# Performance work log

Measured on AMD Instinct MI355X. Metric: run time of the kernel, lower is better.

The kernel has to match this reference:

```python
import jax, jax.numpy as jnp
import numpy as np

L, H, FF, NH = 6, 1024, 4096, 8
HD = H // NH
B, S = 4, 1024
EPS = 1e-5


def _fp8_roundtrip(w):
    # matches torch path: cast to float8_e4m3fn and back (done once at init, no grad)
    return w.astype(jnp.float8_e4m3fn).astype(w.dtype)


def setup_inputs() -> dict:
    key = jax.random.key(0)
    ks = jax.random.split(key, 6)
    x = jax.random.normal(ks[0], (B, S, H), dtype=jnp.float32)
    sH = 1.0 / np.sqrt(H)
    sF = 1.0 / np.sqrt(FF)
    qkv_w = _fp8_roundtrip(jax.random.normal(ks[1], (L, 3 * H, H), jnp.float32) * sH)
    proj_w = _fp8_roundtrip(jax.random.normal(ks[2], (L, H, H), jnp.float32) * sH)
    fc1_w = _fp8_roundtrip(jax.random.normal(ks[3], (L, FF, H), jnp.float32) * sH)
    fc2_w = _fp8_roundtrip(jax.random.normal(ks[4], (L, H, FF), jnp.float32) * sF)
    return {
        "x": x,
        "qkv_w": qkv_w, "qkv_b": jnp.zeros((L, 3 * H), jnp.float32),
        "proj_w": proj_w, "proj_b": jnp.zeros((L, H), jnp.float32),
        "fc1_w": fc1_w, "fc1_b": jnp.zeros((L, FF), jnp.float32),
        "fc2_w": fc2_w, "fc2_b": jnp.zeros((L, H), jnp.float32),
        "ln1_s": jnp.ones((L, H), jnp.float32), "ln1_b": jnp.zeros((L, H), jnp.float32),
        "ln2_s": jnp.ones((L, H), jnp.float32), "ln2_b": jnp.zeros((L, H), jnp.float32),
    }


def _layernorm(x, scale, bias):
    mu = jnp.mean(x, axis=-1, keepdims=True)
    var = jnp.var(x, axis=-1, keepdims=True)
    return (x - mu) / jnp.sqrt(var + EPS) * scale + bias


def reference(x, qkv_w, qkv_b, proj_w, proj_b, fc1_w, fc1_b, fc2_w, fc2_b,
              ln1_s, ln1_b, ln2_s, ln2_b):
    b, s, h = x.shape
    for i in range(L):
        # --- attention block ---
        residual = x
        hx = _layernorm(x, ln1_s[i], ln1_b[i])
        qkv = hx @ qkv_w[i].T + qkv_b[i]                       # [b, s, 3h]
        q, k, v = jnp.split(qkv, 3, axis=-1)
        q = q.reshape(b, s, NH, HD).transpose(0, 2, 1, 3)      # [b, nh, s, hd]
        k = k.reshape(b, s, NH, HD).transpose(0, 2, 1, 3)
        v = v.reshape(b, s, NH, HD).transpose(0, 2, 1, 3)
        scores = jnp.einsum('bhqd,bhkd->bhqk', q, k) / np.sqrt(HD)
        attn = jax.nn.softmax(scores, axis=-1)
        out = jnp.einsum('bhqk,bhkd->bhqd', attn, v)           # [b, nh, s, hd]
        out = out.transpose(0, 2, 1, 3).reshape(b, s, h)
        x = out @ proj_w[i].T + proj_b[i] + residual
        # --- FFN block ---
        residual = x
        hx = _layernorm(x, ln2_s[i], ln2_b[i])
        ff = jax.nn.relu(hx @ fc1_w[i].T + fc1_b[i])
        x = ff @ fc2_w[i].T + fc2_b[i] + residual
    return x
```

## Files before the change

### kernel.cpp

```cpp
#include <hip/hip_runtime.h>
#include <stdint.h>

typedef __bf16 bf16;
typedef __bf16 bf16x4 __attribute__((ext_vector_type(4)));
typedef __bf16 bf16x8 __attribute__((ext_vector_type(8)));
typedef float  f32x4  __attribute__((ext_vector_type(4)));

#define NLAYER 6
#define HDIM   1024
#define FFDIM  4096
#define NHEAD  8
#define HEADD  128
#define SEQ    1024
#define NTOK   4096

__device__ __forceinline__ void g2l16(const void* g, void* l) {
  __builtin_amdgcn_global_load_lds(
      (const __attribute__((address_space(1))) void*)g,
      (__attribute__((address_space(3))) void*)l, 16, 0, 0);
}

__global__ __launch_bounds__(256) void cvt_w(const float* __restrict__ in,
                                             bf16* __restrict__ out, int n8) {
  int i = blockIdx.x * 256 + threadIdx.x;
  if (i >= n8) return;
  const f32x4* p = (const f32x4*)in + (size_t)i * 2;
  f32x4 a = p[0], b = p[1];
  bf16x8 o;
  o[0] = (bf16)a[0]; o[1] = (bf16)a[1]; o[2] = (bf16)a[2]; o[3] = (bf16)a[3];
  o[4] = (bf16)b[0]; o[5] = (bf16)b[1]; o[6] = (bf16)b[2]; o[7] = (bf16)b[3];
  *((bf16x8*)out + i) = o;
}

__global__ __launch_bounds__(256) void ln_k(const float* __restrict__ x,
                                            const float* __restrict__ sc,
                                            const float* __restrict__ bi,
                                            bf16* __restrict__ out) {
  int row = blockIdx.x, t = threadIdx.x;
  f32x4 v = *((const f32x4*)(x + (size_t)row * HDIM) + t);
  float s = v[0] + v[1] + v[2] + v[3];
  float q = v[0]*v[0] + v[1]*v[1] + v[2]*v[2] + v[3]*v[3];
#pragma unroll
  for (int m = 1; m < 64; m <<= 1) {
    s += __shfl_xor(s, m, 64);
    q += __shfl_xor(q, m, 64);
  }
  __shared__ float ss[4], qq[4];
  if ((t & 63) == 0) { ss[t >> 6] = s; qq[t >> 6] = q; }
  __syncthreads();
  s = ss[0] + ss[1] + ss[2] + ss[3];
  q = qq[0] + qq[1] + qq[2] + qq[3];
  float mu  = s * (1.f / HDIM);
  float var = q * (1.f / HDIM) - mu * mu;
  float rs  = rsqrtf(var + 1e-5f);
  f32x4 g = *((const f32x4*)sc + t);
  f32x4 b = *((const f32x4*)bi + t);
  bf16x4 o;
#pragma unroll
  for (int j = 0; j < 4; j++) o[j] = (bf16)((v[j] - mu) * rs * g[j] + b[j]);
  *((bf16x4*)(out + (size_t)row * HDIM) + t) = o;
}

template <bool RELU, bool RESID, bool OUTF32, bool SPLITV>
__global__ __launch_bounds__(256) void gemm5(const bf16* __restrict__ A,
                                             const bf16* __restrict__ W,
                                             const float* __restrict__ bias,
                                             const float* resid, void* outp,
                                             bf16* __restrict__ vt,
                                             int M, int N, int K) {
  __shared__ bf16 As[2][128 * 64];
  __shared__ bf16 Bs[2][128 * 64];
  int tid = threadIdx.x;
  int lane = tid & 63, w = tid >> 6;
  int g = lane >> 4, r = lane & 15;
  int wr = w >> 1, wc = w & 1;
  int nbx = N >> 7;
  int cpx = gridDim.x >> 3;
  int swz = (blockIdx.x & 7) * cpx + (blockIdx.x >> 3);
  int bm = swz / nbx, bn = swz % nbx;
  const bf16* Ab = A + (size_t)bm * 128 * K;
  const bf16* Wb = W + (size_t)bn * 128 * K;
  f32x4 acc[4][4] = {};

  auto STAGE = [&](int buf, int k0) {
#pragma unroll
    for (int i = 0; i < 4; ++i) {
      int c = i * 256 + tid;
      int row = c >> 3;
      int kk = ((c & 7) ^ (row & 7)) << 3;
      g2l16(Ab + (size_t)row * K + k0 + kk, (char*)As[buf] + c * 16);
      g2l16(Wb + (size_t)row * K + k0 + kk, (char*)Bs[buf] + c * 16);
    }
  };
  auto COMPUTE = [&](int buf) {
#pragma unroll
    for (int ks = 0; ks < 2; ++ks) {
      bf16x8 af[4], bfr[4];
#pragma unroll
      for (int mi = 0; mi < 4; mi++) {
        int row = wr * 64 + mi * 16 + r;
        af[mi] = *(const bf16x8*)((const char*)As[buf] + row * 128 +
                                  ((ks * 64 + g * 16) ^ ((row & 7) << 4)));
      }
#pragma unroll
      for (int ni = 0; ni < 4; ni++) {
        int row = wc * 64 + ni * 16 + r;
        bfr[ni] = *(const bf16x8*)((const char*)Bs[buf] + row * 128 +
                                   ((ks * 64 + g * 16) ^ ((row & 7) << 4)));
      }
      __builtin_amdgcn_s_setprio(1);
#pragma unroll
      for (int mi = 0; mi < 4; mi++)
#pragma unroll
        for (int ni = 0; ni < 4; ni++)
          acc[mi][ni] = __builtin_amdgcn_mfma_f32_16x16x32_bf16(
              af[mi], bfr[ni], acc[mi][ni], 0, 0, 0);
      __builtin_amdgcn_s_setprio(0);
    }
  };

  int nt = K >> 6;
  STAGE(0, 0);
  __syncthreads();
  int cur = 0;
  for (int t = 0; t < nt - 1; ++t) {
    STAGE(cur ^ 1, (t + 1) << 6);
    COMPUTE(cur);
    __syncthreads();
    cur ^= 1;
  }
  COMPUTE(cur);

#pragma unroll
  for (int ni = 0; ni < 4; ++ni) {
    int col = bn * 128 + wc * 64 + ni * 16 + r;
    float bv = bias[col];
    bool vpart = SPLITV && (bn * 128 + wc * 64 + ni * 16) >= 2048;
    if (vpart) {
      int hh = (col - 2048) >> 7, dd = col & 127;
#pragma unroll
      for (int mi = 0; mi < 4; ++mi) {
        int row0 = bm * 128 + wr * 64 + mi * 16 + g * 4;
        int bb = row0 >> 10, ss = row0 & 1023;
        bf16x4 o;
#pragma unroll
        for (int j = 0; j < 4; j++) o[j] = (bf16)(acc[mi][ni][j] + bv);
        *(bf16x4*)(vt + ((size_t)((bb * NHEAD + hh) * HEADD + dd)) * SEQ + ss) = o;
      }
    } else {
#pragma unroll
      for (int mi = 0; mi < 4; ++mi) {
        int row0 = bm * 128 + wr * 64 + mi * 16 + g * 4;
#pragma unroll
        for (int j = 0; j < 4; j++) {
          size_t idx = (size_t)(row0 + j) * N + col;
          float v = acc[mi][ni][j] + bv;
          if constexpr (RELU) v = fmaxf(v, 0.f);
          if constexpr (RESID) v += resid[idx];
          if constexpr (OUTF32) ((float*)outp)[idx] = v;
          else                  ((bf16*)outp)[idx] = (bf16)v;
        }
      }
    }
  }
  (void)M;
}

__global__ __launch_bounds__(256) void attn_k(const bf16* __restrict__ qkv,
                                              const bf16* __restrict__ vt,
                                              bf16* __restrict__ out) {
  __shared__ bf16 Ks[64 * 128];
  __shared__ bf16 VT[128 * 64];
  __shared__ bf16 Ps[4][1024];
  int qt = blockIdx.x, h = blockIdx.y, b = blockIdx.z;
  int tid = threadIdx.x, lane = tid & 63, w = tid >> 6;
  int g = lane >> 4, r = lane & 15;
  int q0 = qt * 64;
  size_t tok0 = (size_t)b * SEQ;
  char* psw = (char*)Ps + w * 2048;

  bf16x8 qf[4];
  {
    const bf16* qp = qkv + (tok0 + q0 + w * 16 + r) * 3072 + h * HEADD;
#pragma unroll
    for (int ks = 0; ks < 4; ks++) qf[ks] = *(const bf16x8*)(qp + ks * 32 + g * 8);
  }
  f32x4 oacc[8] = {};
  float mprev[4], lsum[4];
#pragma unroll
  for (int j = 0; j < 4; j++) { mprev[j] = -1e30f; lsum[j] = 0.f; }
  const float scl = 0.08838834764831845f;
  const bf16* vtb = vt + (size_t)(b * NHEAD + h) * HEADD * SEQ;

  for (int c0 = 0; c0 < SEQ; c0 += 64) {
    const bf16* kbase = qkv + (tok0 + c0) * 3072 + 1024 + h * HEADD;
#pragma unroll
    for (int i = 0; i < 4; i++) {
      int cb = i * 256 + w * 64;
      int c  = cb + lane;
      int krow = c >> 4;
      int kkk  = ((c & 15) ^ (krow & 7)) << 3;
      g2l16(kbase + (size_t)krow * 3072 + kkk, (char*)Ks + cb * 16);
      int vrow = c >> 3;
      int vcol = ((c & 7) ^ (vrow & 7)) << 3;
      g2l16(vtb + (size_t)vrow * SEQ + c0 + vcol, (char*)VT + cb * 16);
    }
    __syncthreads();

    f32x4 sacc[4] = {};
#pragma unroll
    for (int ks = 0; ks < 4; ks++) {
#pragma unroll
      for (int cb = 0; cb < 4; cb++) {
        int row = cb * 16 + r;
        bf16x8 kf = *(const bf16x8*)((const char*)Ks + row * 256 +
                                     ((ks * 64 + g * 16) ^ ((row & 7) << 4)));
        sacc[cb] = __builtin_amdgcn_mfma_f32_16x16x32_bf16(qf[ks], kf, sacc[cb], 0, 0, 0);
      }
    }
#pragma unroll
    for (int cb = 0; cb < 4; cb++) {
      sacc[cb][0] *= scl; sacc[cb][1] *= scl; sacc[cb][2] *= scl; sacc[cb][3] *= scl;
    }
    float sf[4];
#pragma unroll
    for (int j = 0; j < 4; j++) {
      float m = fmaxf(fmaxf(sacc[0][j], sacc[1][j]), fmaxf(sacc[2][j], sacc[3][j]));
      m = fmaxf(m, __shfl_xor(m, 1, 64));
      m = fmaxf(m, __shfl_xor(m, 2, 64));
      m = fmaxf(m, __shfl_xor(m, 4, 64));
      m = fmaxf(m, __shfl_xor(m, 8, 64));
      float mn = fmaxf(mprev[j], m);
      float f  = __expf(mprev[j] - mn);
      mprev[j] = mn; sf[j] = f;
      float rs = 0.f;
#pragma unroll
      for (int cb = 0; cb < 4; cb++) {
        float p = __expf(sacc[cb][j] - mn);
        sacc[cb][j] = p; rs += p;
      }
      rs += __shfl_xor(rs, 1, 64);
      rs += __shfl_xor(rs, 2, 64);
      rs += __shfl_xor(rs, 4, 64);
      rs += __shfl_xor(rs, 8, 64);
      lsum[j] = lsum[j] * f + rs;
    }
#pragma unroll
    for (int nb = 0; nb < 8; nb++) {
      oacc[nb][0] *= sf[0]; oacc[nb][1] *= sf[1];
      oacc[nb][2] *= sf[2]; oacc[nb][3] *= sf[3];
    }
#pragma unroll
    for (int cb = 0; cb < 4; cb++) {
      int cbyte = cb * 32 + r * 2;
#pragma unroll
      for (int j = 0; j < 4; j++) {
        int q = g * 4 + j;
        *(bf16*)(psw + q * 128 + (cbyte ^ ((q & 7) << 4))) = (bf16)sacc[cb][j];
      }
    }
    asm volatile("s_waitcnt lgkmcnt(0)" ::: "memory");
    __builtin_amdgcn_sched_barrier(0);
#pragma unroll
    for (int cs = 0; cs < 2; cs++) {
      bf16x8 pf = *(const bf16x8*)(psw + r * 128 + ((cs * 64 + g * 16) ^ ((r & 7) << 4)));
#pragma unroll
      for (int nb = 0; nb < 8; nb++) {
        int vrow = nb * 16 + r;
        bf16x8 vf = *(const bf16x8*)((const char*)VT + vrow * 128 +
                                     ((cs * 64 + g * 16) ^ ((vrow & 7) << 4)));
        oacc[nb] = __builtin_amdgcn_mfma_f32_16x16x32_bf16(pf, vf, oacc[nb], 0, 0, 0);
      }
    }
    __syncthreads();
  }

  float rl[4];
#pragma unroll
  for (int j = 0; j < 4; j++) rl[j] = 1.f / lsum[j];
#pragma unroll
  for (int nb = 0; nb < 8; nb++)
#pragma unroll
    for (int j = 0; j < 4; j++)
      out[(tok0 + q0 + w * 16 + g * 4 + j) * HDIM + h * HEADD + nb * 16 + r] =
          (bf16)(oacc[nb][j] * rl[j]);
}

extern "C" void kernel_launch(void* const* d_in, const int* in_sizes, int n_in,
                              void* d_out, int out_size, void* d_ws, size_t ws_size,
                              hipStream_t stream) {
  const float* x_in   = (const float*)d_in[0];
  const float* qkv_w  = (const float*)d_in[1];
  const float* qkv_b  = (const float*)d_in[2];
  const float* proj_w = (const float*)d_in[3];
  const float* proj_b = (const float*)d_in[4];
  const float* fc1_w  = (const float*)d_in[5];
  const float* fc1_b  = (const float*)d_in[6];
  const float* fc2_w  = (const float*)d_in[7];
  const float* fc2_b  = (const float*)d_in[8];
  const float* ln1_s  = (const float*)d_in[9];
  const float* ln1_b  = (const float*)d_in[10];
  const float* ln2_s  = (const float*)d_in[11];
  const float* ln2_b  = (const float*)d_in[12];

  char* ws = (char*)d_ws;
  size_t o = 0;
  bf16* Wq = (bf16*)(ws + o); o += (size_t)NLAYER * 3 * HDIM * HDIM * 2;
  bf16* Wp = (bf16*)(ws + o); o += (size_t)NLAYER * HDIM * HDIM * 2;
  bf16* W1 = (bf16*)(ws + o); o += (size_t)NLAYER * FFDIM * HDIM * 2;
  bf16* W2 = (bf16*)(ws + o); o += (size_t)NLAYER * HDIM * FFDIM * 2;
  bf16* hx   = (bf16*)(ws + o); o += (size_t)NTOK * HDIM * 2;
  bf16* qkvb = (bf16*)(ws + o); o += (size_t)NTOK * 3 * HDIM * 2;
  bf16* Vt   = (bf16*)(ws + o); o += (size_t)NTOK * HDIM * 2;
  bf16* aout = (bf16*)(ws + o); o += (size_t)NTOK * HDIM * 2;
  bf16* ffb  = (bf16*)(ws + o); o += (size_t)NTOK * FFDIM * 2;
  float* xbuf = (float*)d_out;

  {
    int n8;
    n8 = NLAYER * 3 * HDIM * HDIM / 8;
    cvt_w<<<(n8 + 255) / 256, 256, 0, stream>>>(qkv_w, Wq, n8);
    n8 = NLAYER * HDIM * HDIM / 8;
    cvt_w<<<(n8 + 255) / 256, 256, 0, stream>>>(proj_w, Wp, n8);
    n8 = NLAYER * FFDIM * HDIM / 8;
    cvt_w<<<(n8 + 255) / 256, 256, 0, stream>>>(fc1_w, W1, n8);
    n8 = NLAYER * HDIM * FFDIM / 8;
    cvt_w<<<(n8 + 255) / 256, 256, 0, stream>>>(fc2_w, W2, n8);
  }

  for (int i = 0; i < NLAYER; i++) {
    const float* xc = (i == 0) ? x_in : xbuf;
    ln_k<<<NTOK, 256, 0, stream>>>(xc, ln1_s + i * HDIM, ln1_b + i * HDIM, hx);
    gemm5<false, false, false, true><<<(NTOK / 128) * (3 * HDIM / 128), 256, 0, stream>>>(
        hx, Wq + (size_t)i * 3 * HDIM * HDIM, qkv_b + i * 3 * HDIM, nullptr,
        qkvb, Vt, NTOK, 3 * HDIM, HDIM);
    attn_k<<<dim3(SEQ / 64, NHEAD, 4), 256, 0, stream>>>(qkvb, Vt, aout);
    gemm5<false, true, true, false><<<(NTOK / 128) * (HDIM / 128), 256, 0, stream>>>(
        aout, Wp + (size_t)i * HDIM * HDIM, proj_b + i * HDIM, xc,
        xbuf, nullptr, NTOK, HDIM, HDIM);
    ln_k<<<NTOK, 256, 0, stream>>>(xbuf, ln2_s + i * HDIM, ln2_b + i * HDIM, hx);
    gemm5<true, false, false, false><<<(NTOK / 128) * (FFDIM / 128), 256, 0, stream>>>(
        hx, W1 + (size_t)i * FFDIM * HDIM, fc1_b + i * FFDIM, nullptr,
        ffb, nullptr, NTOK, FFDIM, HDIM);
    gemm5<false, true, true, false><<<(NTOK / 128) * (HDIM / 128), 256, 0, stream>>>(
        ffb, W2 + (size_t)i * HDIM * FFDIM, fc2_b + i * HDIM, xbuf,
        xbuf, nullptr, NTOK, HDIM, FFDIM);
  }
  (void)in_sizes; (void)n_in; (void)out_size; (void)ws_size;
}
```

Measured before the change: 1.835 ms.

## Split GEMM K dimension across two warp groups within a block

The GEMM block grows to 512 threads, and each 256-thread half processes half of the K range with its own double-buffered LDS tiles. The two partial accumulators are then reduced through LDS, and only the first half runs the epilogue. The goal is more waves per tile to hide latency, especially for small-grid GEMMs like the proj and fc2 launches. In exchange, LDS use doubles to 128KB per block, occupancy drops, and the reduction and epilogue add serialized work.

Result: no change. 1.808 ms (-1.4%).

```diff
diff --git a/kernel.cpp b/kernel.cpp
--- a/kernel.cpp
+++ b/kernel.cpp
@@ -62,18 +62,21 @@
 }
 
 template <bool RELU, bool RESID, bool OUTF32, bool SPLITV>
-__global__ __launch_bounds__(256) void gemm5(const bf16* __restrict__ A,
-                                             const bf16* __restrict__ W,
-                                             const float* __restrict__ bias,
-                                             const float* resid, void* outp,
-                                             bf16* __restrict__ vt,
-                                             int M, int N, int K) {
-  __shared__ bf16 As[2][128 * 64];
-  __shared__ bf16 Bs[2][128 * 64];
+__global__ __launch_bounds__(512) void gemmsk(const bf16* __restrict__ A,
+                                              const bf16* __restrict__ W,
+                                              const float* __restrict__ bias,
+                                              const float* resid, void* outp,
+                                              bf16* __restrict__ vt,
+                                              int M, int N, int K) {
+  __shared__ bf16 As[2][2][128 * 64];
+  __shared__ bf16 Bs[2][2][128 * 64];
   int tid = threadIdx.x;
-  int lane = tid & 63, w = tid >> 6;
+  int gr = tid >> 8;
+  int gtid = tid & 255;
+  int lane = tid & 63;
+  int w4 = gtid >> 6;
   int g = lane >> 4, r = lane & 15;
-  int wr = w >> 1, wc = w & 1;
+  int wr = w4 >> 1, wc = w4 & 1;
   int nbx = N >> 7;
   int cpx = gridDim.x >> 3;
   int swz = (blockIdx.x & 7) * cpx + (blockIdx.x >> 3);
@@ -85,11 +88,11 @@
   auto STAGE = [&](int buf, int k0) {
 #pragma unroll
     for (int i = 0; i < 4; ++i) {
-      int c = i * 256 + tid;
+      int c = i * 256 + gtid;
       int row = c >> 3;
       int kk = ((c & 7) ^ (row & 7)) << 3;
-      g2l16(Ab + (size_t)row * K + k0 + kk, (char*)As[buf] + c * 16);
-      g2l16(Wb + (size_t)row * K + k0 + kk, (char*)Bs[buf] + c * 16);
+      g2l16(Ab + (size_t)row * K + k0 + kk, (char*)As[gr][buf] + c * 16);
+      g2l16(Wb + (size_t)row * K + k0 + kk, (char*)Bs[gr][buf] + c * 16);
     }
   };
   auto COMPUTE = [&](int buf) {
@@ -99,13 +102,13 @@
 #pragma unroll
       for (int mi = 0; mi < 4; mi++) {
         int row = wr * 64 + mi * 16 + r;
-        af[mi] = *(const bf16x8*)((const char*)As[buf] + row * 128 +
+        af[mi] = *(const bf16x8*)((const char*)As[gr][buf] + row * 128 +
                                   ((ks * 64 + g * 16) ^ ((row & 7) << 4)));
       }
 #pragma unroll
       for (int ni = 0; ni < 4; ni++) {
         int row = wc * 64 + ni * 16 + r;
-        bfr[ni] = *(const bf16x8*)((const char*)Bs[buf] + row * 128 +
+        bfr[ni] = *(const bf16x8*)((const char*)Bs[gr][buf] + row * 128 +
                                    ((ks * 64 + g * 16) ^ ((row & 7) << 4)));
       }
       __builtin_amdgcn_s_setprio(1);
@@ -119,46 +122,65 @@
     }
   };
 
-  int nt = K >> 6;
-  STAGE(0, 0);
+  int kbase = gr * (K >> 1);
+  int nt = K >> 7;
+  STAGE(0, kbase);
   __syncthreads();
   int cur = 0;
   for (int t = 0; t < nt - 1; ++t) {
-    STAGE(cur ^ 1, (t + 1) << 6);
+    STAGE(cur ^ 1, kbase + ((t + 1) << 6));
     COMPUTE(cur);
     __syncthreads();
     cur ^= 1;
   }
   COMPUTE(cur);
 
-#pragma unroll
-  for (int ni = 0; ni < 4; ++ni) {
-    int col = bn * 128 + wc * 64 + ni * 16 + r;
-    float bv = bias[col];
-    bool vpart = SPLITV && (bn * 128 + wc * 64 + ni * 16) >= 2048;
-    if (vpart) {
-      int hh = (col - 2048) >> 7, dd = col & 127;
-#pragma unroll
-      for (int mi = 0; mi < 4; ++mi) {
-        int row0 = bm * 128 + wr * 64 + mi * 16 + g * 4;
-        int bb = row0 >> 10, ss = row0 & 1023;
-        bf16x4 o;
-#pragma unroll
-        for (int j = 0; j < 4; j++) o[j] = (bf16)(acc[mi][ni][j] + bv);
-        *(bf16x4*)(vt + ((size_t)((bb * NHEAD + hh) * HEADD + dd)) * SEQ + ss) = o;
-      }
-    } else {
-#pragma unroll
-      for (int mi = 0; mi < 4; ++mi) {
-        int row0 = bm * 128 + wr * 64 + mi * 16 + g * 4;
-#pragma unroll
-        for (int j = 0; j < 4; j++) {
-          size_t idx = (size_t)(row0 + j) * N + col;
-          float v = acc[mi][ni][j] + bv;
-          if constexpr (RELU) v = fmaxf(v, 0.f);
-          if constexpr (RESID) v += resid[idx];
-          if constexpr (OUTF32) ((float*)outp)[idx] = v;
-          else                  ((bf16*)outp)[idx] = (bf16)v;
+  __syncthreads();
+  f32x4* red = (f32x4*)As;
+  if (gr == 1) {
+#pragma unroll
+    for (int mi = 0; mi < 4; mi++)
+#pragma unroll
+      for (int ni = 0; ni < 4; ni++)
+        red[(w4 * 64 + lane) * 16 + mi * 4 + ni] = acc[mi][ni];
+  }
+  __syncthreads();
+  if (gr == 0) {
+#pragma unroll
+    for (int mi = 0; mi < 4; mi++)
+#pragma unroll
+      for (int ni = 0; ni < 4; ni++)
+        acc[mi][ni] += red[(w4 * 64 + lane) * 16 + mi * 4 + ni];
+
+#pragma unroll
+    for (int ni = 0; ni < 4; ++ni) {
+      int col = bn * 128 + wc * 64 + ni * 16 + r;
+      float bv = bias[col];
+      bool vpart = SPLITV && (bn * 128 + wc * 64 + ni * 16) >= 2048;
+      if (vpart) {
+        int hh = (col - 2048) >> 7, dd = col & 127;
+#pragma unroll
+        for (int mi = 0; mi < 4; ++mi) {
+          int row0 = bm * 128 + wr * 64 + mi * 16 + g * 4;
+          int bb = row0 >> 10, ss = row0 & 1023;
+          bf16x4 o;
+#pragma unroll
+          for (int j = 0; j < 4; j++) o[j] = (bf16)(acc[mi][ni][j] + bv);
+          *(bf16x4*)(vt + ((size_t)((bb * NHEAD + hh) * HEADD + dd)) * SEQ + ss) = o;
+        }
+      } else {
+#pragma unroll
+        for (int mi = 0; mi < 4; ++mi) {
+          int row0 = bm * 128 + wr * 64 + mi * 16 + g * 4;
+#pragma unroll
+          for (int j = 0; j < 4; j++) {
+            size_t idx = (size_t)(row0 + j) * N + col;
+            float v = acc[mi][ni][j] + bv;
+            if constexpr (RELU) v = fmaxf(v, 0.f);
+            if constexpr (RESID) v += resid[idx];
+            if constexpr (OUTF32) ((float*)outp)[idx] = v;
+            else                  ((bf16*)outp)[idx] = (bf16)v;
+          }
         }
       }
     }
@@ -331,18 +353,18 @@
   for (int i = 0; i < NLAYER; i++) {
     const float* xc = (i == 0) ? x_in : xbuf;
     ln_k<<<NTOK, 256, 0, stream>>>(xc, ln1_s + i * HDIM, ln1_b + i * HDIM, hx);
-    gemm5<false, false, false, true><<<(NTOK / 128) * (3 * HDIM / 128), 256, 0, stream>>>(
+    gemmsk<false, false, false, true><<<(NTOK / 128) * (3 * HDIM / 128), 512, 0, stream>>>(
         hx, Wq + (size_t)i * 3 * HDIM * HDIM, qkv_b + i * 3 * HDIM, nullptr,
         qkvb, Vt, NTOK, 3 * HDIM, HDIM);
     attn_k<<<dim3(SEQ / 64, NHEAD, 4), 256, 0, stream>>>(qkvb, Vt, aout);
-    gemm5<false, true, true, false><<<(NTOK / 128) * (HDIM / 128), 256, 0, stream>>>(
+    gemmsk<false, true, true, false><<<(NTOK / 128) * (HDIM / 128), 512, 0, stream>>>(
         aout, Wp + (size_t)i * HDIM * HDIM, proj_b + i * HDIM, xc,
         xbuf, nullptr, NTOK, HDIM, HDIM);
     ln_k<<<NTOK, 256, 0, stream>>>(xbuf, ln2_s + i * HDIM, ln2_b + i * HDIM, hx);
-    gemm5<true, false, false, false><<<(NTOK / 128) * (FFDIM / 128), 256, 0, stream>>>(
+    gemmsk<true, false, false, false><<<(NTOK / 128) * (FFDIM / 128), 512, 0, stream>>>(
         hx, W1 + (size_t)i * FFDIM * HDIM, fc1_b + i * FFDIM, nullptr,
         ffb, nullptr, NTOK, FFDIM, HDIM);
-    gemm5<false, true, true, false><<<(NTOK / 128) * (HDIM / 128), 256, 0, stream>>>(
+    gemmsk<false, true, true, false><<<(NTOK / 128) * (HDIM / 128), 512, 0, stream>>>(
         ffb, W2 + (size_t)i * HDIM * FFDIM, fc2_b + i * HDIM, xbuf,
         xbuf, nullptr, NTOK, HDIM, FFDIM);
   }
```

## Use 512-thread 256-row GEMM tiles with triple-buffered async LDS pipeline

Applied to the files above, without the earlier changes.

Replaces the 128x128 double-buffered GEMM with a templated kernel using 8 waves, 256-row M tiles, a BN of 128 or 64 depending on N, and a three-stage LDS ring. Each stage waits on vmcnt and then a barrier, so a stage can be loaded while another is being computed and there is one barrier per iteration. This aims to raise the MFMA-to-load ratio, hide global latency, and keep enough blocks for the narrow N=1024 GEMMs. In exchange it uses more LDS, which may lower occupancy, and it depends on hand-written vmcnt counts being correct.

New measurement: 1.648 ms. 1.11x faster.

```diff
diff --git a/kernel.cpp b/kernel.cpp
--- a/kernel.cpp
+++ b/kernel.cpp
@@ -61,58 +61,66 @@
   *((bf16x4*)(out + (size_t)row * HDIM) + t) = o;
 }
 
-template <bool RELU, bool RESID, bool OUTF32, bool SPLITV>
-__global__ __launch_bounds__(256) void gemm5(const bf16* __restrict__ A,
-                                             const bf16* __restrict__ W,
-                                             const float* __restrict__ bias,
-                                             const float* resid, void* outp,
-                                             bf16* __restrict__ vt,
-                                             int M, int N, int K) {
-  __shared__ bf16 As[2][128 * 64];
-  __shared__ bf16 Bs[2][128 * 64];
+template <int BN, bool RELU, bool RESID, bool OUTF32, bool SPLITV>
+__global__ __launch_bounds__(512) void gemm8p(const bf16* __restrict__ A,
+                                              const bf16* __restrict__ W,
+                                              const float* __restrict__ bias,
+                                              const float* resid, void* outp,
+                                              bf16* __restrict__ vt,
+                                              int N, int K) {
+  constexpr int NI  = BN / 32;
+  constexpr int BCH = BN * 8;
+  __shared__ bf16 As[3][256 * 64];
+  __shared__ bf16 Bs[3][BN * 64];
   int tid = threadIdx.x;
   int lane = tid & 63, w = tid >> 6;
   int g = lane >> 4, r = lane & 15;
   int wr = w >> 1, wc = w & 1;
-  int nbx = N >> 7;
+  int nbx = N / BN;
   int cpx = gridDim.x >> 3;
   int swz = (blockIdx.x & 7) * cpx + (blockIdx.x >> 3);
   int bm = swz / nbx, bn = swz % nbx;
-  const bf16* Ab = A + (size_t)bm * 128 * K;
-  const bf16* Wb = W + (size_t)bn * 128 * K;
-  f32x4 acc[4][4] = {};
-
-  auto STAGE = [&](int buf, int k0) {
+  const bf16* Ab = A + (size_t)bm * 256 * K;
+  const bf16* Wb = W + (size_t)bn * BN * K;
+  f32x4 acc[4][NI] = {};
+
+  auto STAGE = [&](char* aB, char* bB, int k0) {
 #pragma unroll
     for (int i = 0; i < 4; ++i) {
-      int c = i * 256 + tid;
+      int c = i * 512 + tid;
       int row = c >> 3;
       int kk = ((c & 7) ^ (row & 7)) << 3;
-      g2l16(Ab + (size_t)row * K + k0 + kk, (char*)As[buf] + c * 16);
-      g2l16(Wb + (size_t)row * K + k0 + kk, (char*)Bs[buf] + c * 16);
+      g2l16(Ab + (size_t)row * K + k0 + kk, aB + c * 16);
+    }
+#pragma unroll
+    for (int i = 0; i < BCH / 512; ++i) {
+      int c = i * 512 + tid;
+      int row = c >> 3;
+      int kk = ((c & 7) ^ (row & 7)) << 3;
+      g2l16(Wb + (size_t)row * K + k0 + kk, bB + c * 16);
     }
   };
-  auto COMPUTE = [&](int buf) {
+  auto COMPUTE = [&](const char* aB, const char* bB) {
 #pragma unroll
     for (int ks = 0; ks < 2; ++ks) {
-      bf16x8 af[4], bfr[4];
+      bf16x8 af[4], bfr[NI];
 #pragma unroll
       for (int mi = 0; mi < 4; mi++) {
         int row = wr * 64 + mi * 16 + r;
-        af[mi] = *(const bf16x8*)((const char*)As[buf] + row * 128 +
+        af[mi] = *(const bf16x8*)(aB + row * 128 +
                                   ((ks * 64 + g * 16) ^ ((row & 7) << 4)));
       }
 #pragma unroll
-      for (int ni = 0; ni < 4; ni++) {
-        int row = wc * 64 + ni * 16 + r;
-        bfr[ni] = *(const bf16x8*)((const char*)Bs[buf] + row * 128 +
+      for (int ni = 0; ni < NI; ni++) {
+        int row = wc * (BN / 2) + ni * 16 + r;
+        bfr[ni] = *(const bf16x8*)(bB + row * 128 +
                                    ((ks * 64 + g * 16) ^ ((row & 7) << 4)));
       }
       __builtin_amdgcn_s_setprio(1);
 #pragma unroll
       for (int mi = 0; mi < 4; mi++)
 #pragma unroll
-        for (int ni = 0; ni < 4; ni++)
+        for (int ni = 0; ni < NI; ni++)
           acc[mi][ni] = __builtin_amdgcn_mfma_f32_16x16x32_bf16(
               af[mi], bfr[ni], acc[mi][ni], 0, 0, 0);
       __builtin_amdgcn_s_setprio(0);
@@ -120,27 +128,39 @@
   };
 
   int nt = K >> 6;
-  STAGE(0, 0);
-  __syncthreads();
-  int cur = 0;
-  for (int t = 0; t < nt - 1; ++t) {
-    STAGE(cur ^ 1, (t + 1) << 6);
-    COMPUTE(cur);
-    __syncthreads();
-    cur ^= 1;
-  }
-  COMPUTE(cur);
-
-#pragma unroll
-  for (int ni = 0; ni < 4; ++ni) {
-    int col = bn * 128 + wc * 64 + ni * 16 + r;
+  char *a0 = (char*)As[0], *a1 = (char*)As[1], *a2 = (char*)As[2];
+  char *b0 = (char*)Bs[0], *b1 = (char*)Bs[1], *b2 = (char*)Bs[2];
+  STAGE(a0, b0, 0);
+  STAGE(a1, b1, 64);
+  for (int t = 0; t < nt - 2; ++t) {
+    if constexpr (BN == 128) asm volatile("s_waitcnt vmcnt(6)" ::: "memory");
+    else                     asm volatile("s_waitcnt vmcnt(5)" ::: "memory");
+    __builtin_amdgcn_s_barrier();
+    STAGE(a2, b2, (t + 2) << 6);
+    COMPUTE(a0, b0);
+    char* x;
+    x = a0; a0 = a1; a1 = a2; a2 = x;
+    x = b0; b0 = b1; b1 = b2; b2 = x;
+  }
+  if constexpr (BN == 128) asm volatile("s_waitcnt vmcnt(6)" ::: "memory");
+  else                     asm volatile("s_waitcnt vmcnt(5)" ::: "memory");
+  __builtin_amdgcn_s_barrier();
+  COMPUTE(a0, b0);
+  asm volatile("s_waitcnt vmcnt(0)" ::: "memory");
+  __builtin_amdgcn_s_barrier();
+  COMPUTE(a1, b1);
+
+#pragma unroll
+  for (int ni = 0; ni < NI; ++ni) {
+    int cbase = bn * BN + wc * (BN / 2) + ni * 16;
+    int col = cbase + r;
     float bv = bias[col];
-    bool vpart = SPLITV && (bn * 128 + wc * 64 + ni * 16) >= 2048;
+    bool vpart = SPLITV && cbase >= 2048;
     if (vpart) {
       int hh = (col - 2048) >> 7, dd = col & 127;
 #pragma unroll
       for (int mi = 0; mi < 4; ++mi) {
-        int row0 = bm * 128 + wr * 64 + mi * 16 + g * 4;
+        int row0 = bm * 256 + wr * 64 + mi * 16 + g * 4;
         int bb = row0 >> 10, ss = row0 & 1023;
         bf16x4 o;
 #pragma unroll
@@ -150,7 +170,7 @@
     } else {
 #pragma unroll
       for (int mi = 0; mi < 4; ++mi) {
-        int row0 = bm * 128 + wr * 64 + mi * 16 + g * 4;
+        int row0 = bm * 256 + wr * 64 + mi * 16 + g * 4;
 #pragma unroll
         for (int j = 0; j < 4; j++) {
           size_t idx = (size_t)(row0 + j) * N + col;
@@ -163,7 +183,6 @@
       }
     }
   }
-  (void)M;
 }
 
 __global__ __launch_bounds__(256) void attn_k(const bf16* __restrict__ qkv,
@@ -331,20 +350,24 @@
   for (int i = 0; i < NLAYER; i++) {
     const float* xc = (i == 0) ? x_in : xbuf;
     ln_k<<<NTOK, 256, 0, stream>>>(xc, ln1_s + i * HDIM, ln1_b + i * HDIM, hx);
-    gemm5<false, false, false, true><<<(NTOK / 128) * (3 * HDIM / 128), 256, 0, stream>>>(
+    gemm8p<128, false, false, false, true>
+        <<<(NTOK / 256) * (3 * HDIM / 128), 512, 0, stream>>>(
         hx, Wq + (size_t)i * 3 * HDIM * HDIM, qkv_b + i * 3 * HDIM, nullptr,
-        qkvb, Vt, NTOK, 3 * HDIM, HDIM);
+        qkvb, Vt, 3 * HDIM, HDIM);
     attn_k<<<dim3(SEQ / 64, NHEAD, 4), 256, 0, stream>>>(qkvb, Vt, aout);
-    gemm5<false, true, true, false><<<(NTOK / 128) * (HDIM / 128), 256, 0, stream>>>(
+    gemm8p<64, false, true, true, false>
+        <<<(NTOK / 256) * (HDIM / 64), 512, 0, stream>>>(
         aout, Wp + (size_t)i * HDIM * HDIM, proj_b + i * HDIM, xc,
-        xbuf, nullptr, NTOK, HDIM, HDIM);
+        xbuf, nullptr, HDIM, HDIM);
     ln_k<<<NTOK, 256, 0, stream>>>(xbuf, ln2_s + i * HDIM, ln2_b + i * HDIM, hx);
-    gemm5<true, false, false, false><<<(NTOK / 128) * (FFDIM / 128), 256, 0, stream>>>(
+    gemm8p<128, true, false, false, false>
+        <<<(NTOK / 256) * (FFDIM / 128), 512, 0, stream>>>(
         hx, W1 + (size_t)i * FFDIM * HDIM, fc1_b + i * FFDIM, nullptr,
-        ffb, nullptr, NTOK, FFDIM, HDIM);
-    gemm5<false, true, true, false><<<(NTOK / 128) * (HDIM / 128), 256, 0, stream>>>(
+        ffb, nullptr, FFDIM, HDIM);
+    gemm8p<64, false, true, true, false>
+        <<<(NTOK / 256) * (HDIM / 64), 512, 0, stream>>>(
         ffb, W2 + (size_t)i * HDIM * FFDIM, fc2_b + i * HDIM, xbuf,
-        xbuf, nullptr, NTOK, HDIM, FFDIM);
+        xbuf, nullptr, HDIM, FFDIM);
   }
   (void)in_sizes; (void)n_in; (void)out_size; (void)ws_size;
 }
```
